# Kernel tuning notes

Hardware: AMD Instinct MI355X
Metric: run time of the kernel (lower is better)

## Reference

```python
import jax, jax.numpy as jnp
import numpy as np

B, S, H = 2, 2048, 2048
NH, NKV = 16, 4
HD = H // NH            # 128
GROUPS = NH // NKV      # 4
ROTARY_BASE = 10000.0
NEG = -1e9


def setup_inputs() -> dict:
    key = jax.random.key(0)
    ks = jax.random.split(key, 6)
    x = jax.random.normal(ks[0], (B, S, H), dtype=jnp.float32)
    # additive causal mask [B,1,S,S]
    causal = jnp.where(jnp.tril(jnp.ones((S, S), dtype=bool)), 0.0, NEG).astype(jnp.float32)
    attention_mask = jnp.broadcast_to(causal[None, None], (B, 1, S, S))
    position_ids = jnp.broadcast_to(jnp.arange(S, dtype=jnp.int32)[None], (B, S))
    sc = 0.02
    Wq = jax.random.normal(ks[1], (H, NH * HD), dtype=jnp.float32) * sc
    Wk = jax.random.normal(ks[2], (H, NKV * HD), dtype=jnp.float32) * sc
    Wv = jax.random.normal(ks[3], (H, NKV * HD), dtype=jnp.float32) * sc
    Wo = jax.random.normal(ks[4], (H, H), dtype=jnp.float32) * sc
    return {"x": x, "attention_mask": attention_mask, "position_ids": position_ids,
            "Wq": Wq, "Wk": Wk, "Wv": Wv, "Wo": Wo}


def _rotate_half(t):
    t1, t2 = t[..., : HD // 2], t[..., HD // 2:]
    return jnp.concatenate((-t2, t1), axis=-1)


def _rope_sin_cos(position_ids, dtype):
    inv_freq = 1.0 / (ROTARY_BASE ** (jnp.arange(0, HD, 2, dtype=jnp.float32) / HD))  # [HD/2]
    freqs = position_ids.astype(jnp.float32)[..., None] * inv_freq[None, None, :]      # [B,S,HD/2]
    emb = jnp.concatenate((freqs, freqs), axis=-1)                                     # [B,S,HD]
    return jnp.sin(emb).astype(dtype), jnp.cos(emb).astype(dtype)


def reference(x, attention_mask, position_ids, Wq, Wk, Wv, Wo):
    # QKV projections (no bias)
    q = (x @ Wq).reshape(B, S, NH, HD).transpose(0, 2, 1, 3)     # [B,NH,S,HD]
    k = (x @ Wk).reshape(B, S, NKV, HD).transpose(0, 2, 1, 3)    # [B,NKV,S,HD]
    v = (x @ Wv).reshape(B, S, NKV, HD).transpose(0, 2, 1, 3)
    sin, cos = _rope_sin_cos(position_ids, x.dtype)
    sin, cos = sin[:, None], cos[:, None]                         # unsqueeze head dim
    q = q * cos + _rotate_half(q) * sin
    k = k * cos + _rotate_half(k) * sin
    # GQA: repeat kv heads
    k = jnp.repeat(k, GROUPS, axis=1)                             # [B,NH,S,HD]
    v = jnp.repeat(v, GROUPS, axis=1)
    scores = jnp.einsum('bhqd,bhkd->bhqk', q, k) / jnp.sqrt(jnp.asarray(HD, x.dtype))
    scores = scores + attention_mask                              # additive causal mask
    attn = jax.nn.softmax(scores.astype(jnp.float32), axis=-1).astype(x.dtype)
    # dropout p=0.0 -> no-op
    out = jnp.einsum('bhqk,bhkd->bhqd', attn, v)                  # [B,NH,S,HD]
    out = out.transpose(0, 2, 1, 3).reshape(B, S, H)
    return out @ Wo
```

## Files before the change

### kernel.cpp

```cpp
#include <hip/hip_runtime.h>
#include <hip/hip_bf16.h>
#include <stdint.h>
#include <math.h>

#define B_ 2
#define S_ 2048
#define H_ 2048
#define NH_ 16
#define NKV_ 4
#define HD_ 128

typedef __bf16 bf16;
typedef __bf16 bf16x8 __attribute__((ext_vector_type(8)));
typedef __bf16 bf16x4 __attribute__((ext_vector_type(4)));
typedef float f32x4 __attribute__((ext_vector_type(4)));

__device__ __forceinline__ void async_copy16(const void* g, void* l) {
  __builtin_amdgcn_global_load_lds(
      (const __attribute__((address_space(1))) void*)(uintptr_t)g,
      (__attribute__((address_space(3))) void*)(uintptr_t)l,
      16, 0, 0);
}

__device__ __forceinline__ f32x4 mfma16(bf16x8 a, bf16x8 b, f32x4 c) {
  return __builtin_amdgcn_mfma_f32_16x16x32_bf16(a, b, c, 0, 0, 0);
}


__global__ void f32_to_bf16_k(const float* __restrict__ in, bf16* __restrict__ o, int n) {
  int i = (blockIdx.x * 256 + threadIdx.x) * 4;
  if (i >= n) return;
  float4 v = *(const float4*)(in + i);
  bf16x4 r;
  r[0] = (bf16)v.x; r[1] = (bf16)v.y; r[2] = (bf16)v.z; r[3] = (bf16)v.w;
  *(bf16x4*)(o + i) = r;
}

__global__ void transpose_to_bf16_k(const float* __restrict__ W, bf16* __restrict__ Wt,
                                    int K, int N) {
  __shared__ float tile[32][33];
  int n0 = blockIdx.x * 32, k0 = blockIdx.y * 32;
  int tx = threadIdx.x, ty = threadIdx.y;
#pragma unroll
  for (int j = 0; j < 32; j += 8)
    tile[ty + j][tx] = W[(size_t)(k0 + ty + j) * N + n0 + tx];
  __syncthreads();
#pragma unroll
  for (int j = 0; j < 32; j += 8)
    Wt[(size_t)(n0 + ty + j) * K + k0 + tx] = (bf16)tile[tx][ty + j];
}

__global__ void rope_table_k(float2* __restrict__ tab) {
  int i = blockIdx.x * 256 + threadIdx.x;
  int p = i >> 6, d = i & 63;
  float invf = expf(-((float)(2 * d) / 128.0f) * 9.210340371976184f);
  float fr = (float)p * invf;
  float sv, cv;
  sincosf(fr, &sv, &cv);
  tab[i] = make_float2(cv, sv);
}

__global__ void rope_apply_k(bf16* __restrict__ t, const int* __restrict__ pos_ids,
                             const float2* __restrict__ tab, int hshift, int hmask,
                             float scale) {
  int i = blockIdx.x * 256 + threadIdx.x;
  int d = i & 63;
  int tmp = i >> 6;
  int h = tmp & hmask;
  int row = tmp >> hshift;
  int pos = pos_ids[row];
  float2 cs = tab[pos * 64 + d];
  size_t base = (((size_t)row << hshift) + h) * HD_;
  float a = (float)t[base + d];
  float b = (float)t[base + d + 64];
  t[base + d]      = (bf16)((a * cs.x - b * cs.y) * scale);
  t[base + d + 64] = (bf16)((b * cs.x + a * cs.y) * scale);
}


template <int MODE>
__global__ __launch_bounds__(512) void gemm256_k(const bf16* __restrict__ A,
                                                 const bf16* __restrict__ Bt,
                                                 void* __restrict__ C0,
                                                 void* __restrict__ C1,
                                                 void* __restrict__ C2,
                                                 int M, int N, int K) {
  extern __shared__ __align__(16) char smem[];
  const int tid = threadIdx.x;
  const int lane = tid & 63;
  const int w = tid >> 6;
  const int wm = w >> 2;
  const int wn = w & 3;
  const int g16 = lane >> 4, c16 = lane & 15;
  const int row0 = blockIdx.y * 256;
  const int col0 = blockIdx.x * 256;
  const int srow = tid >> 3;
  const int sslot = tid & 7;
  const int ldsw = w * 1024;

  auto stage = [&](int buf, int kt, int r) {
    int row = (r & 3) * 64 + srow;
    int ss = sslot ^ (row & 7);
    const bf16* src = (r < 4) ? (A + (size_t)(row0 + row) * K)
                              : (Bt + (size_t)(col0 + row) * K);
    async_copy16(src + (kt << 6) + ss * 8,
                 smem + buf * 65536 + (r >> 2) * 32768 + (r & 3) * 8192 + ldsw);
  };

  int offA[2][8], offB[2][4];
#pragma unroll
  for (int ks = 0; ks < 2; ++ks) {
#pragma unroll
    for (int i = 0; i < 8; ++i) {
      int ra = wm * 128 + i * 16 + c16;
      offA[ks][i] = ra * 128 + (((ks * 4 + g16) ^ (ra & 7)) << 4);
    }
#pragma unroll
    for (int j = 0; j < 4; ++j) {
      int rb = wn * 64 + j * 16 + c16;
      offB[ks][j] = 32768 + rb * 128 + (((ks * 4 + g16) ^ (rb & 7)) << 4);
    }
  }

  const f32x4 fz = {0.f, 0.f, 0.f, 0.f};
  f32x4 acc[8][4];
#pragma unroll
  for (int i = 0; i < 8; ++i)
#pragma unroll
    for (int j = 0; j < 4; ++j) acc[i][j] = fz;

  const int nkt = K >> 6;
#pragma unroll
  for (int r = 0; r < 8; ++r) stage(0, 0, r);
  asm volatile("s_waitcnt vmcnt(0)" ::: "memory");
  __builtin_amdgcn_s_barrier();

  for (int t = 0; t < nkt; ++t) {
    const char* Ab = smem + (t & 1) * 65536;
    const bool pf = (t + 1 < nkt);
    const int nb = (t + 1) & 1;
    bf16x8 bfr[2][4];

    {
      bf16x8 af[2][2];
#pragma unroll
      for (int ks = 0; ks < 2; ++ks) {
#pragma unroll
        for (int j = 0; j < 4; ++j) bfr[ks][j] = *(const bf16x8*)(Ab + offB[ks][j]);
        af[ks][0] = *(const bf16x8*)(Ab + offA[ks][0]);
        af[ks][1] = *(const bf16x8*)(Ab + offA[ks][1]);
      }
      if (pf) { stage(nb, t + 1, 0); stage(nb, t + 1, 1); stage(nb, t + 1, 2); stage(nb, t + 1, 3); }
      __builtin_amdgcn_s_barrier();
      asm volatile("s_waitcnt lgkmcnt(0)" ::: "memory");
      __builtin_amdgcn_sched_barrier(0);
      __builtin_amdgcn_s_setprio(1);
#pragma unroll
      for (int ks = 0; ks < 2; ++ks)
#pragma unroll
        for (int m = 0; m < 2; ++m)
#pragma unroll
          for (int j = 0; j < 4; ++j)
            acc[m][j] = mfma16(af[ks][m], bfr[ks][j], acc[m][j]);
      __builtin_amdgcn_s_setprio(0);
      __builtin_amdgcn_sched_barrier(0);
      __builtin_amdgcn_s_barrier();
    }

#pragma unroll
    for (int q = 1; q < 4; ++q) {
      bf16x8 af[2][2];
#pragma unroll
      for (int ks = 0; ks < 2; ++ks) {
        af[ks][0] = *(const bf16x8*)(Ab + offA[ks][q * 2]);
        af[ks][1] = *(const bf16x8*)(Ab + offA[ks][q * 2 + 1]);
      }
      if (q == 1 && pf) { stage(nb, t + 1, 4); stage(nb, t + 1, 5); stage(nb, t + 1, 6); stage(nb, t + 1, 7); }
      __builtin_amdgcn_s_barrier();
      asm volatile("s_waitcnt lgkmcnt(0)" ::: "memory");
      __builtin_amdgcn_sched_barrier(0);
      __builtin_amdgcn_s_setprio(1);
#pragma unroll
      for (int ks = 0; ks < 2; ++ks)
#pragma unroll
        for (int m = 0; m < 2; ++m)
#pragma unroll
          for (int j = 0; j < 4; ++j)
            acc[q * 2 + m][j] = mfma16(af[ks][m], bfr[ks][j], acc[q * 2 + m][j]);
      __builtin_amdgcn_s_setprio(0);
      __builtin_amdgcn_sched_barrier(0);
      if (q == 3 && pf) asm volatile("s_waitcnt vmcnt(0)" ::: "memory");
      __builtin_amdgcn_s_barrier();
    }
  }

#pragma unroll
  for (int i = 0; i < 8; ++i) {
    int gr0 = row0 + wm * 128 + i * 16 + g16 * 4;
#pragma unroll
    for (int j = 0; j < 4; ++j) {
      int gc = col0 + wn * 64 + j * 16 + c16;
      if constexpr (MODE == 2) {
        if (col0 < 2048) {
#pragma unroll
          for (int r = 0; r < 4; ++r)
            ((bf16*)C0)[(size_t)(gr0 + r) * 2048 + gc] = (bf16)acc[i][j][r];
        } else if (col0 < 2560) {
#pragma unroll
          for (int r = 0; r < 4; ++r)
            ((bf16*)C1)[(size_t)(gr0 + r) * 512 + (gc - 2048)] = (bf16)acc[i][j][r];
        } else {
          int dv = gc - 2560;
          int hkv = dv >> 7, d = dv & 127;
          size_t va = (((size_t)(gr0 >> 11) * NKV_ + hkv) * HD_ + d) * S_ + (gr0 & 2047);
          bf16x4 pk;
#pragma unroll
          for (int r = 0; r < 4; ++r) pk[r] = (bf16)acc[i][j][r];
          *(bf16x4*)((bf16*)C2 + va) = pk;
        }
      } else {
#pragma unroll
        for (int r = 0; r < 4; ++r) {
          if constexpr (MODE == 1)
            ((float*)C0)[(size_t)(gr0 + r) * N + gc] = acc[i][j][r];
          else
            ((bf16*)C0)[(size_t)(gr0 + r) * N + gc] = (bf16)acc[i][j][r];
        }
      }
    }
  }
}


template <int MODE>
__global__ __launch_bounds__(512) void gemm8_k(const bf16* __restrict__ A,
                                               const bf16* __restrict__ Bt,
                                               void* __restrict__ C0,
                                               void* __restrict__ C1,
                                               void* __restrict__ C2,
                                               int M, int N, int K) {
  extern __shared__ __align__(16) char smem[];
  const int tid = threadIdx.x;
  const int lane = tid & 63;
  const int w = tid >> 6;
  const int wm = w >> 2;
  const int wn = w & 3;
  const int g16 = lane >> 4, c16 = lane & 15;
  const int row0 = blockIdx.y * 128;
  const int col0 = blockIdx.x * 256;
  const int srow = tid >> 3;
  const int sslot = tid & 7;
  const int ldsw = w * 1024;

  auto stageA = [&](int s, int kt, int r) {
    int row = r * 64 + srow;
    int ss = sslot ^ (row & 7);
    async_copy16(A + (size_t)(row0 + row) * K + (kt << 6) + ss * 8,
                 smem + s * 49152 + r * 8192 + ldsw);
  };
  auto stageB = [&](int s, int kt, int r) {
    int row = r * 64 + srow;
    int ss = sslot ^ (row & 7);
    async_copy16(Bt + (size_t)(col0 + row) * K + (kt << 6) + ss * 8,
                 smem + s * 49152 + 16384 + r * 8192 + ldsw);
  };

  int offA[2][4], offB[2][4];
#pragma unroll
  for (int ks = 0; ks < 2; ++ks) {
#pragma unroll
    for (int i = 0; i < 4; ++i) {
      int ra = wm * 64 + i * 16 + c16;
      offA[ks][i] = ra * 128 + (((ks * 4 + g16) ^ (ra & 7)) << 4);
      int rb = wn * 64 + i * 16 + c16;
      offB[ks][i] = rb * 128 + (((ks * 4 + g16) ^ (rb & 7)) << 4);
    }
  }

  const f32x4 fz = {0.f, 0.f, 0.f, 0.f};
  f32x4 acc[4][4];
#pragma unroll
  for (int i = 0; i < 4; ++i)
#pragma unroll
    for (int j = 0; j < 4; ++j) acc[i][j] = fz;

  const int nkt = K >> 6;
#pragma unroll
  for (int r = 0; r < 2; ++r) stageA(0, 0, r);
#pragma unroll
  for (int r = 0; r < 4; ++r) stageB(0, 0, r);
#pragma unroll
  for (int r = 0; r < 2; ++r) stageA(1, 1, r);
#pragma unroll
  for (int r = 0; r < 4; ++r) stageB(1, 1, r);
  asm volatile("s_waitcnt vmcnt(6)" ::: "memory");
  __builtin_amdgcn_s_barrier();

  int ct = 0, pt = 2;
  for (int t = 0; t < nkt; ++t) {
    const char* Ab = smem + ct * 49152;
    const char* Bb = Ab + 16384;
    const bool pf = (t + 2 < nkt);
    const int kpf = t + 2;
    bf16x8 af[4], bfr[4];

#pragma unroll
    for (int i = 0; i < 4; ++i) af[i] = *(const bf16x8*)(Ab + offA[0][i]);
#pragma unroll
    for (int j = 0; j < 4; ++j) bfr[j] = *(const bf16x8*)(Bb + offB[0][j]);
    if (pf) { stageA(pt, kpf, 0); stageA(pt, kpf, 1); stageB(pt, kpf, 0); }
    __builtin_amdgcn_s_barrier();
    asm volatile("s_waitcnt lgkmcnt(0)" ::: "memory");
    __builtin_amdgcn_sched_barrier(0);
    __builtin_amdgcn_s_setprio(1);
#pragma unroll
    for (int i = 0; i < 4; ++i)
#pragma unroll
      for (int j = 0; j < 4; ++j) acc[i][j] = mfma16(af[i], bfr[j], acc[i][j]);
    __builtin_amdgcn_s_setprio(0);
    __builtin_amdgcn_sched_barrier(0);
    __builtin_amdgcn_s_barrier();

#pragma unroll
    for (int i = 0; i < 4; ++i) af[i] = *(const bf16x8*)(Ab + offA[1][i]);
#pragma unroll
    for (int j = 0; j < 4; ++j) bfr[j] = *(const bf16x8*)(Bb + offB[1][j]);
    if (pf) { stageB(pt, kpf, 1); stageB(pt, kpf, 2); stageB(pt, kpf, 3); }
    if (pf) asm volatile("s_waitcnt vmcnt(6)" ::: "memory");
    else    asm volatile("s_waitcnt vmcnt(0)" ::: "memory");
    __builtin_amdgcn_s_barrier();
    asm volatile("s_waitcnt lgkmcnt(0)" ::: "memory");
    __builtin_amdgcn_sched_barrier(0);
    __builtin_amdgcn_s_setprio(1);
#pragma unroll
    for (int i = 0; i < 4; ++i)
#pragma unroll
      for (int j = 0; j < 4; ++j) acc[i][j] = mfma16(af[i], bfr[j], acc[i][j]);
    __builtin_amdgcn_s_setprio(0);
    __builtin_amdgcn_sched_barrier(0);
    __builtin_amdgcn_s_barrier();

    ct = (ct == 2) ? 0 : ct + 1;
    pt = (pt == 2) ? 0 : pt + 1;
  }

#pragma unroll
  for (int i = 0; i < 4; ++i) {
    int gr0 = row0 + wm * 64 + i * 16 + g16 * 4;
#pragma unroll
    for (int j = 0; j < 4; ++j) {
      int gc = col0 + wn * 64 + j * 16 + c16;
#pragma unroll
      for (int r = 0; r < 4; ++r) {
        if constexpr (MODE == 1)
          ((float*)C0)[(size_t)(gr0 + r) * N + gc] = acc[i][j][r];
        else
          ((bf16*)C0)[(size_t)(gr0 + r) * N + gc] = (bf16)acc[i][j][r];
      }
    }
  }
}


template <bool OUT_F32, bool VT_Z1>
__global__ __launch_bounds__(256) void gemm_bt_k(const bf16* __restrict__ A,
                                                 const bf16* __restrict__ Bt0,
                                                 const bf16* __restrict__ Bt1,
                                                 void* __restrict__ C0, void* __restrict__ C1,
                                                 int M, int N, int K) {
  const bf16* __restrict__ Bt = (blockIdx.z == 0) ? Bt0 : Bt1;
  void* C = (blockIdx.z == 0) ? C0 : C1;
  __shared__ __align__(16) bf16 As[128 * 64];
  __shared__ __align__(16) bf16 Bs[128 * 64];
  const int tid = threadIdx.x;
  const int lane = tid & 63;
  const int w = tid >> 6;
  const int wm = w >> 1, wn = w & 1;
  const int g16 = lane >> 4, c16 = lane & 15;
  const int row0 = blockIdx.y * 128;
  const int col0 = blockIdx.x * 128;
  const int sr = lane >> 3;
  const int st = lane & 7;
  const int ss = st ^ sr;

  const f32x4 fz = {0.f, 0.f, 0.f, 0.f};
  f32x4 acc[4][4];
#pragma unroll
  for (int i = 0; i < 4; ++i)
#pragma unroll
    for (int j = 0; j < 4; ++j) acc[i][j] = fz;

  const int nkt = K >> 6;
  for (int kt = 0; kt < nkt; ++kt) {
    const int k0 = kt << 6;
    __syncthreads();
#pragma unroll
    for (int c = 0; c < 4; ++c) {
      int rbase = w * 32 + c * 8;
      async_copy16(A + (size_t)(row0 + rbase + sr) * K + k0 + ss * 8,
                   (char*)As + rbase * 128);
      async_copy16(Bt + (size_t)(col0 + rbase + sr) * K + k0 + ss * 8,
                   (char*)Bs + rbase * 128);
    }
    __syncthreads();
#pragma unroll
    for (int ks = 0; ks < 2; ++ks) {
      bf16x8 af[4], bfr[4];
#pragma unroll
      for (int t = 0; t < 4; ++t) {
        int ra = wm * 64 + t * 16 + c16;
        af[t] = *(const bf16x8*)((const char*)As + ra * 128 + (((ks * 4 + g16) ^ (ra & 7)) << 4));
        int rb = wn * 64 + t * 16 + c16;
        bfr[t] = *(const bf16x8*)((const char*)Bs + rb * 128 + (((ks * 4 + g16) ^ (rb & 7)) << 4));
      }
#pragma unroll
      for (int i = 0; i < 4; ++i)
#pragma unroll
        for (int j = 0; j < 4; ++j) acc[i][j] = mfma16(af[i], bfr[j], acc[i][j]);
    }
  }

  const bool vt = VT_Z1 && (blockIdx.z == 1);
#pragma unroll
  for (int i = 0; i < 4; ++i) {
    int gr0 = row0 + wm * 64 + i * 16 + g16 * 4;
#pragma unroll
    for (int j = 0; j < 4; ++j) {
      int gc = col0 + wn * 64 + j * 16 + c16;
      if (vt) {
        size_t va = ((size_t)((gr0 >> 11) * NKV_ + (gc >> 7)) * HD_ + (gc & 127)) * S_ + (gr0 & 2047);
        bf16x4 pk;
#pragma unroll
        for (int r = 0; r < 4; ++r) pk[r] = (bf16)acc[i][j][r];
        *(bf16x4*)((bf16*)C + va) = pk;
      } else {
#pragma unroll
        for (int r = 0; r < 4; ++r) {
          if constexpr (OUT_F32)
            ((float*)C)[(size_t)(gr0 + r) * N + gc] = acc[i][j][r];
          else
            ((bf16*)C)[(size_t)(gr0 + r) * N + gc] = (bf16)acc[i][j][r];
        }
      }
    }
  }
}


__global__ __launch_bounds__(256, 2) void attn_fwd_k(const bf16* __restrict__ Qg,
                                                     const bf16* __restrict__ Kg,
                                                     const bf16* __restrict__ VTg,
                                                     bf16* __restrict__ Og) {
  __shared__ __align__(16) bf16 Ks[2][64 * 128];
  __shared__ __align__(16) bf16 Vt[2][128 * 64];

  const int tid = threadIdx.x;
  const int lane = tid & 63;
  const int w = tid >> 6;
  const int g16 = lane >> 4;
  const int c16 = lane & 15;

  int bid = blockIdx.x;
  int rr_ = bid >> 5, bh = bid & 31;
  int qb = (rr_ < 8) ? (15 - rr_) : (rr_ - 8);
  const int b = bh >> 4;
  const int h = bh & 15;
  const int hkv = h >> 2;
  const int q0 = qb * 128;
  const int qw = q0 + w * 32;

  bf16x8 qf[2][4];
#pragma unroll
  for (int nq = 0; nq < 2; ++nq)
#pragma unroll
    for (int ksq = 0; ksq < 4; ++ksq)
      qf[nq][ksq] = *(const bf16x8*)(Qg + ((size_t)(b * S_ + qw + nq * 16 + c16) * NH_ + h) * HD_ + (ksq * 4 + g16) * 8);

  float m_run[2] = {-1e30f, -1e30f};
  float l_run[2] = {0.f, 0.f};
  const f32x4 fz = {0.f, 0.f, 0.f, 0.f};
  f32x4 acc[2][8];
#pragma unroll
  for (int nq = 0; nq < 2; ++nq)
#pragma unroll
    for (int dt = 0; dt < 8; ++dt) acc[nq][dt] = fz;

  const size_t kbase = ((size_t)b * S_ * NKV_ + hkv) * HD_;
  const size_t vbase = ((size_t)(b * NKV_ + hkv)) * HD_ * S_;

  auto stage = [&](int buf, int kv0) {
#pragma unroll
    for (int rd = 0; rd < 4; ++rd) {
      int Lb = rd * 256 + w * 64;
      int row = (Lb + lane) >> 4;
      int ssl = (lane & 15) ^ (row & 7);
      async_copy16(Kg + kbase + (size_t)(kv0 + row) * (NKV_ * HD_) + ssl * 8,
                   (char*)&Ks[buf][0] + Lb * 16);
    }
#pragma unroll
    for (int rd = 0; rd < 4; ++rd) {
      int Lb = rd * 256 + w * 64;
      int row = (Lb + lane) >> 3;
      int ssl = (lane & 7) ^ (row & 7);
      async_copy16(VTg + vbase + (size_t)row * S_ + kv0 + ssl * 8,
                   (char*)&Vt[buf][0] + Lb * 16);
    }
  };

  const int ntiles = 2 * qb + 2;
  stage(0, 0);
  int cur = 0;

  for (int t = 0; t < ntiles; ++t) {
    __syncthreads();
    if (t + 1 < ntiles) stage(cur ^ 1, (t + 1) * 64);
    const int kv0 = t * 64;

    if (kv0 <= qw + 31) {
      const bf16* KsC = &Ks[cur][0];
      const bf16* VtC = &Vt[cur][0];

      f32x4 sc[2][4];
#pragma unroll
      for (int nq = 0; nq < 2; ++nq)
#pragma unroll
        for (int mt = 0; mt < 4; ++mt) sc[nq][mt] = fz;

      __builtin_amdgcn_s_setprio(1);
#pragma unroll
      for (int ksq = 0; ksq < 4; ++ksq) {
        bf16x8 kf[4];
#pragma unroll
        for (int mt = 0; mt < 4; ++mt) {
          int gp = c16 >> 2, rp = c16 & 3;
          int blk = 8 * (mt >> 1) + 2 * gp + ((mt & 1) ^ (gp & 1));
          int row = blk * 4 + rp;
          kf[mt] = *(const bf16x8*)((const char*)KsC + row * 256 + (((ksq * 4 + g16) ^ (row & 7)) << 4));
        }
#pragma unroll
        for (int nq = 0; nq < 2; ++nq)
#pragma unroll
          for (int mt = 0; mt < 4; ++mt)
            sc[nq][mt] = mfma16(kf[mt], qf[nq][ksq], sc[nq][mt]);
      }
      __builtin_amdgcn_s_setprio(0);

      if (kv0 + 63 > qw) {
#pragma unroll
        for (int nq = 0; nq < 2; ++nq) {
          int qa = qw + nq * 16 + c16;
#pragma unroll
          for (int mt = 0; mt < 4; ++mt) {
            int blk = 8 * (mt >> 1) + 2 * g16 + ((mt & 1) ^ (g16 & 1));
#pragma unroll
            for (int r = 0; r < 4; ++r) {
              int ka = kv0 + blk * 4 + r;
              if (ka > qa) sc[nq][mt][r] = -1e30f;
            }
          }
        }
      }

      float mx[2];
#pragma unroll
      for (int nq = 0; nq < 2; ++nq) {
        float v = sc[nq][0][0];
#pragma unroll
        for (int mt = 0; mt < 4; ++mt)
#pragma unroll
          for (int r = 0; r < 4; ++r) v = fmaxf(v, sc[nq][mt][r]);
        v = fmaxf(v, __shfl_xor(v, 16));
        v = fmaxf(v, __shfl_xor(v, 32));
        mx[nq] = v;
      }
      if (__any((mx[0] > m_run[0] + 8.f) || (mx[1] > m_run[1] + 8.f))) {
#pragma unroll
        for (int nq = 0; nq < 2; ++nq) {
          float mn = fmaxf(m_run[nq], mx[nq]);
          float corr = exp2f(m_run[nq] - mn);
          m_run[nq] = mn;
          l_run[nq] *= corr;
#pragma unroll
          for (int dt = 0; dt < 8; ++dt) acc[nq][dt] *= corr;
        }
      }
#pragma unroll
      for (int nq = 0; nq < 2; ++nq) {
        float sum = 0.f;
#pragma unroll
        for (int mt = 0; mt < 4; ++mt)
#pragma unroll
          for (int r = 0; r < 4; ++r) {
            float p = exp2f(sc[nq][mt][r] - m_run[nq]);
            sc[nq][mt][r] = p;
            sum += p;
          }
        sum += __shfl_xor(sum, 16);
        sum += __shfl_xor(sum, 32);
        l_run[nq] += sum;
      }

      bf16x8 pa[2][2];
#pragma unroll
      for (int nq = 0; nq < 2; ++nq)
#pragma unroll
        for (int ks = 0; ks < 2; ++ks) {
          f32x4 sA = (g16 & 1) ? sc[nq][2 * ks + 1] : sc[nq][2 * ks];
          f32x4 sB = (g16 & 1) ? sc[nq][2 * ks] : sc[nq][2 * ks + 1];
          bf16x8 tf;
          tf[0] = (bf16)sA[0]; tf[1] = (bf16)sA[1]; tf[2] = (bf16)sA[2]; tf[3] = (bf16)sA[3];
          tf[4] = (bf16)sB[0]; tf[5] = (bf16)sB[1]; tf[6] = (bf16)sB[2]; tf[7] = (bf16)sB[3];
          pa[nq][ks] = tf;
        }

      __builtin_amdgcn_s_setprio(1);
#pragma unroll
      for (int ks = 0; ks < 2; ++ks)
#pragma unroll
        for (int dt = 0; dt < 8; ++dt) {
          int rv = dt * 16 + c16;
          bf16x8 vf = *(const bf16x8*)((const char*)VtC + rv * 128 + (((ks * 4 + g16) ^ (rv & 7)) << 4));
          acc[0][dt] = mfma16(vf, pa[0][ks], acc[0][dt]);
          acc[1][dt] = mfma16(vf, pa[1][ks], acc[1][dt]);
        }
      __builtin_amdgcn_s_setprio(0);
    }
    cur ^= 1;
  }

#pragma unroll
  for (int nq = 0; nq < 2; ++nq) {
    float inv = 1.0f / l_run[nq];
    size_t base = ((size_t)(b * S_ + qw + nq * 16 + c16) * NH_ + h) * HD_ + g16 * 4;
#pragma unroll
    for (int dt = 0; dt < 8; ++dt) {
      bf16x4 ov;
#pragma unroll
      for (int r = 0; r < 4; ++r) ov[r] = (bf16)(acc[nq][dt][r] * inv);
      *(bf16x4*)(Og + base + dt * 16) = ov;
    }
  }
}


extern "C" void kernel_launch(void* const* d_in, const int* in_sizes, int n_in,
                              void* d_out, int out_size, void* d_ws, size_t ws_size,
                              hipStream_t stream) {
  const float* x  = (const float*)d_in[0];
  const int* pos  = (const int*)d_in[2];
  const float* Wq = (const float*)d_in[3];
  const float* Wk = (const float*)d_in[4];
  const float* Wv = (const float*)d_in[5];
  const float* Wo = (const float*)d_in[6];

  char* ws = (char*)d_ws;
  size_t off = 0;
  auto alloc = [&](size_t bytes) -> char* {
    char* p = ws + off;
    off += (bytes + 255) & ~(size_t)255;
    return p;
  };
  const size_t rows = (size_t)B_ * S_;
  bf16* xb    = (bf16*)alloc(rows * H_ * 2);
  bf16* bq    = (bf16*)alloc(rows * (NH_ * HD_) * 2);
  bf16* batt  = (bf16*)alloc(rows * (NH_ * HD_) * 2);
  bf16* WqkvT = (bf16*)alloc((size_t)3072 * H_ * 2);
  bf16* WoT   = (bf16*)alloc((size_t)H_ * H_ * 2);
  bf16* bk    = (bf16*)alloc(rows * (NKV_ * HD_) * 2);
  bf16* VT    = (bf16*)alloc(rows * (NKV_ * HD_) * 2);
  float2* tab = (float2*)alloc((size_t)S_ * 64 * sizeof(float2));

  bf16* WqT = WqkvT;
  bf16* WkT = WqkvT + (size_t)2048 * H_;
  bf16* WvT = WqkvT + (size_t)2560 * H_;

  auto* fqkv = gemm256_k<2>;
  auto* fo   = gemm8_k<1>;
  const int lds256 = 2 * 65536;
  const int lds8   = 3 * 49152;
  bool big =
      (hipFuncSetAttribute((const void*)fqkv, hipFuncAttributeMaxDynamicSharedMemorySize, lds256) == hipSuccess) &&
      (hipFuncSetAttribute((const void*)fo, hipFuncAttributeMaxDynamicSharedMemorySize, lds8) == hipSuccess);

  f32_to_bf16_k<<<(rows * H_) / (256 * 4), 256, 0, stream>>>(x, xb, rows * H_);
  transpose_to_bf16_k<<<dim3(H_ / 32, H_ / 32), dim3(32, 8), 0, stream>>>(Wq, WqT, H_, NH_ * HD_);
  transpose_to_bf16_k<<<dim3((NKV_ * HD_) / 32, H_ / 32), dim3(32, 8), 0, stream>>>(Wk, WkT, H_, NKV_ * HD_);
  transpose_to_bf16_k<<<dim3((NKV_ * HD_) / 32, H_ / 32), dim3(32, 8), 0, stream>>>(Wv, WvT, H_, NKV_ * HD_);
  transpose_to_bf16_k<<<dim3(H_ / 32, H_ / 32), dim3(32, 8), 0, stream>>>(Wo, WoT, H_, H_);
  rope_table_k<<<(S_ * 64) / 256, 256, 0, stream>>>(tab);

  if (big) {
    gemm256_k<2><<<dim3(12, 16), 512, lds256, stream>>>(xb, WqkvT, bq, bk, VT, 4096, 3072, 2048);
  } else {
    gemm_bt_k<false, false><<<dim3(16, 32, 1), 256, 0, stream>>>(xb, WqT, WqT, bq, bq, 4096, 2048, 2048);
    gemm_bt_k<false, true><<<dim3(4, 32, 2), 256, 0, stream>>>(xb, WkT, WvT, bk, VT, 4096, 512, 2048);
  }

  rope_apply_k<<<(4096 * NH_ * 64) / 256, 256, 0, stream>>>(bq, pos, tab, 4, 15, 0.12753102f);
  rope_apply_k<<<(4096 * NKV_ * 64) / 256, 256, 0, stream>>>(bk, pos, tab, 2, 3, 1.0f);

  attn_fwd_k<<<dim3(512), 256, 0, stream>>>(bq, bk, VT, batt);

  if (big)
    gemm8_k<1><<<dim3(8, 32), 512, lds8, stream>>>(batt, WoT, d_out, nullptr, nullptr, 4096, 2048, 2048);
  else
    gemm_bt_k<true, false><<<dim3(16, 32, 1), 256, 0, stream>>>(batt, WoT, WoT, d_out, d_out, 4096, 2048, 2048);
}
```

Before: 212.5 us.

## Merge weight transposes, vectorize RoPE, retile QKV GEMM, software-pipeline attention PV

The four weight-transpose launches become one kernel that dispatches on block index. RoPE application is vectorized to 8 bf16 elements per thread. The QKV GEMM is templated on N-tile width and now uses 192-column tiles, giving a 16x16 grid instead of 12x16 for better CU fill. The attention kernel gains a third V buffer and defers each tile's PV MFMAs until after the next tile's QK MFMAs, so softmax latency overlaps with matrix work. The fallback small-GEMM path is removed, which assumes large dynamic LDS is always available.

```diff
diff --git a/kernel.cpp b/kernel.cpp
--- a/kernel.cpp
+++ b/kernel.cpp
@@ -36,10 +36,18 @@
   *(bf16x4*)(o + i) = r;
 }
 
-__global__ void transpose_to_bf16_k(const float* __restrict__ W, bf16* __restrict__ Wt,
-                                    int K, int N) {
+__global__ void transpose_all_k(const float* __restrict__ Wq, const float* __restrict__ Wk,
+                                const float* __restrict__ Wv, const float* __restrict__ Wo,
+                                bf16* __restrict__ WqkvT, bf16* __restrict__ WoT) {
   __shared__ float tile[32][33];
-  int n0 = blockIdx.x * 32, k0 = blockIdx.y * 32;
+  int bid = blockIdx.x;
+  const float* W; bf16* Wt; int N, bx, by;
+  if (bid < 4096)      { W = Wq; Wt = WqkvT;                          N = 2048; int b2 = bid;        bx = b2 & 63; by = b2 >> 6; }
+  else if (bid < 5120) { W = Wk; Wt = WqkvT + (size_t)2048 * 2048;    N = 512;  int b2 = bid - 4096; bx = b2 & 15; by = b2 >> 4; }
+  else if (bid < 6144) { W = Wv; Wt = WqkvT + (size_t)2560 * 2048;    N = 512;  int b2 = bid - 5120; bx = b2 & 15; by = b2 >> 4; }
+  else                 { W = Wo; Wt = WoT;                            N = 2048; int b2 = bid - 6144; bx = b2 & 63; by = b2 >> 6; }
+  const int K = 2048;
+  int n0 = bx * 32, k0 = by * 32;
   int tx = threadIdx.x, ty = threadIdx.y;
 #pragma unroll
   for (int j = 0; j < 32; j += 8)
@@ -60,25 +68,41 @@
   tab[i] = make_float2(cv, sv);
 }
 
-__global__ void rope_apply_k(bf16* __restrict__ t, const int* __restrict__ pos_ids,
-                             const float2* __restrict__ tab, int hshift, int hmask,
-                             float scale) {
+__global__ void rope_apply_v8_k(bf16* __restrict__ t, const int* __restrict__ pos_ids,
+                                const float2* __restrict__ tab, int hshift, int hmask,
+                                float scale) {
   int i = blockIdx.x * 256 + threadIdx.x;
-  int d = i & 63;
-  int tmp = i >> 6;
+  int g = i & 7;
+  int tmp = i >> 3;
   int h = tmp & hmask;
   int row = tmp >> hshift;
   int pos = pos_ids[row];
-  float2 cs = tab[pos * 64 + d];
-  size_t base = (((size_t)row << hshift) + h) * HD_;
-  float a = (float)t[base + d];
-  float b = (float)t[base + d + 64];
-  t[base + d]      = (bf16)((a * cs.x - b * cs.y) * scale);
-  t[base + d + 64] = (bf16)((b * cs.x + a * cs.y) * scale);
-}
-
-
-template <int MODE>
+  size_t base = (((size_t)row << hshift) + h) * HD_ + g * 8;
+  const float2* tb = tab + pos * 64 + g * 8;
+  bf16x8 lo = *(const bf16x8*)(t + base);
+  bf16x8 hi = *(const bf16x8*)(t + base + 64);
+  float4 t0 = *(const float4*)(tb);
+  float4 t1 = *(const float4*)(tb + 2);
+  float4 t2 = *(const float4*)(tb + 4);
+  float4 t3 = *(const float4*)(tb + 6);
+  float cs[8], sn[8];
+  cs[0]=t0.x; sn[0]=t0.y; cs[1]=t0.z; sn[1]=t0.w;
+  cs[2]=t1.x; sn[2]=t1.y; cs[3]=t1.z; sn[3]=t1.w;
+  cs[4]=t2.x; sn[4]=t2.y; cs[5]=t2.z; sn[5]=t2.w;
+  cs[6]=t3.x; sn[6]=t3.y; cs[7]=t3.z; sn[7]=t3.w;
+  bf16x8 olo, ohi;
+#pragma unroll
+  for (int j = 0; j < 8; ++j) {
+    float a = (float)lo[j], b = (float)hi[j];
+    olo[j] = (bf16)((a * cs[j] - b * sn[j]) * scale);
+    ohi[j] = (bf16)((b * cs[j] + a * sn[j]) * scale);
+  }
+  *(bf16x8*)(t + base) = olo;
+  *(bf16x8*)(t + base + 64) = ohi;
+}
+
+
+template <int MODE, int NJ>
 __global__ __launch_bounds__(512) void gemm256_k(const bf16* __restrict__ A,
                                                  const bf16* __restrict__ Bt,
                                                  void* __restrict__ C0,
@@ -86,6 +110,7 @@
                                                  void* __restrict__ C2,
                                                  int M, int N, int K) {
   extern __shared__ __align__(16) char smem[];
+  constexpr int BUFSZ = 32768 + NJ * 8192;
   const int tid = threadIdx.x;
   const int lane = tid & 63;
   const int w = tid >> 6;
@@ -93,21 +118,22 @@
   const int wn = w & 3;
   const int g16 = lane >> 4, c16 = lane & 15;
   const int row0 = blockIdx.y * 256;
-  const int col0 = blockIdx.x * 256;
+  const int col0 = blockIdx.x * (NJ * 64);
   const int srow = tid >> 3;
   const int sslot = tid & 7;
   const int ldsw = w * 1024;
 
   auto stage = [&](int buf, int kt, int r) {
-    int row = (r & 3) * 64 + srow;
+    int rr = (r < 4) ? r : r - 4;
+    int row = rr * 64 + srow;
     int ss = sslot ^ (row & 7);
     const bf16* src = (r < 4) ? (A + (size_t)(row0 + row) * K)
                               : (Bt + (size_t)(col0 + row) * K);
     async_copy16(src + (kt << 6) + ss * 8,
-                 smem + buf * 65536 + (r >> 2) * 32768 + (r & 3) * 8192 + ldsw);
+                 smem + buf * BUFSZ + ((r < 4) ? 0 : 32768) + rr * 8192 + ldsw);
   };
 
-  int offA[2][8], offB[2][4];
+  int offA[2][8], offB[2][NJ];
 #pragma unroll
   for (int ks = 0; ks < 2; ++ks) {
 #pragma unroll
@@ -116,37 +142,37 @@
       offA[ks][i] = ra * 128 + (((ks * 4 + g16) ^ (ra & 7)) << 4);
     }
 #pragma unroll
-    for (int j = 0; j < 4; ++j) {
-      int rb = wn * 64 + j * 16 + c16;
+    for (int j = 0; j < NJ; ++j) {
+      int rb = wn * (16 * NJ) + j * 16 + c16;
       offB[ks][j] = 32768 + rb * 128 + (((ks * 4 + g16) ^ (rb & 7)) << 4);
     }
   }
 
   const f32x4 fz = {0.f, 0.f, 0.f, 0.f};
-  f32x4 acc[8][4];
+  f32x4 acc[8][NJ];
 #pragma unroll
   for (int i = 0; i < 8; ++i)
 #pragma unroll
-    for (int j = 0; j < 4; ++j) acc[i][j] = fz;
+    for (int j = 0; j < NJ; ++j) acc[i][j] = fz;
 
   const int nkt = K >> 6;
 #pragma unroll
-  for (int r = 0; r < 8; ++r) stage(0, 0, r);
+  for (int r = 0; r < 4 + NJ; ++r) stage(0, 0, r);
   asm volatile("s_waitcnt vmcnt(0)" ::: "memory");
   __builtin_amdgcn_s_barrier();
 
   for (int t = 0; t < nkt; ++t) {
-    const char* Ab = smem + (t & 1) * 65536;
+    const char* Ab = smem + (t & 1) * BUFSZ;
     const bool pf = (t + 1 < nkt);
     const int nb = (t + 1) & 1;
-    bf16x8 bfr[2][4];
+    bf16x8 bfr[2][NJ];
 
     {
       bf16x8 af[2][2];
 #pragma unroll
       for (int ks = 0; ks < 2; ++ks) {
 #pragma unroll
-        for (int j = 0; j < 4; ++j) bfr[ks][j] = *(const bf16x8*)(Ab + offB[ks][j]);
+        for (int j = 0; j < NJ; ++j) bfr[ks][j] = *(const bf16x8*)(Ab + offB[ks][j]);
         af[ks][0] = *(const bf16x8*)(Ab + offA[ks][0]);
         af[ks][1] = *(const bf16x8*)(Ab + offA[ks][1]);
       }
@@ -160,7 +186,7 @@
 #pragma unroll
         for (int m = 0; m < 2; ++m)
 #pragma unroll
-          for (int j = 0; j < 4; ++j)
+          for (int j = 0; j < NJ; ++j)
             acc[m][j] = mfma16(af[ks][m], bfr[ks][j], acc[m][j]);
       __builtin_amdgcn_s_setprio(0);
       __builtin_amdgcn_sched_barrier(0);
@@ -175,7 +201,10 @@
         af[ks][0] = *(const bf16x8*)(Ab + offA[ks][q * 2]);
         af[ks][1] = *(const bf16x8*)(Ab + offA[ks][q * 2 + 1]);
       }
-      if (q == 1 && pf) { stage(nb, t + 1, 4); stage(nb, t + 1, 5); stage(nb, t + 1, 6); stage(nb, t + 1, 7); }
+      if (q == 1 && pf) {
+#pragma unroll
+        for (int r = 0; r < NJ; ++r) stage(nb, t + 1, 4 + r);
+      }
       __builtin_amdgcn_s_barrier();
       asm volatile("s_waitcnt lgkmcnt(0)" ::: "memory");
       __builtin_amdgcn_sched_barrier(0);
@@ -185,7 +214,7 @@
 #pragma unroll
         for (int m = 0; m < 2; ++m)
 #pragma unroll
-          for (int j = 0; j < 4; ++j)
+          for (int j = 0; j < NJ; ++j)
             acc[q * 2 + m][j] = mfma16(af[ks][m], bfr[ks][j], acc[q * 2 + m][j]);
       __builtin_amdgcn_s_setprio(0);
       __builtin_amdgcn_sched_barrier(0);
@@ -198,14 +227,14 @@
   for (int i = 0; i < 8; ++i) {
     int gr0 = row0 + wm * 128 + i * 16 + g16 * 4;
 #pragma unroll
-    for (int j = 0; j < 4; ++j) {
-      int gc = col0 + wn * 64 + j * 16 + c16;
+    for (int j = 0; j < NJ; ++j) {
+      int gc = col0 + wn * (16 * NJ) + j * 16 + c16;
       if constexpr (MODE == 2) {
-        if (col0 < 2048) {
+        if (gc < 2048) {
 #pragma unroll
           for (int r = 0; r < 4; ++r)
             ((bf16*)C0)[(size_t)(gr0 + r) * 2048 + gc] = (bf16)acc[i][j][r];
-        } else if (col0 < 2560) {
+        } else if (gc < 2560) {
 #pragma unroll
           for (int r = 0; r < 4; ++r)
             ((bf16*)C1)[(size_t)(gr0 + r) * 512 + (gc - 2048)] = (bf16)acc[i][j][r];
@@ -362,97 +391,12 @@
 }
 
 
-template <bool OUT_F32, bool VT_Z1>
-__global__ __launch_bounds__(256) void gemm_bt_k(const bf16* __restrict__ A,
-                                                 const bf16* __restrict__ Bt0,
-                                                 const bf16* __restrict__ Bt1,
-                                                 void* __restrict__ C0, void* __restrict__ C1,
-                                                 int M, int N, int K) {
-  const bf16* __restrict__ Bt = (blockIdx.z == 0) ? Bt0 : Bt1;
-  void* C = (blockIdx.z == 0) ? C0 : C1;
-  __shared__ __align__(16) bf16 As[128 * 64];
-  __shared__ __align__(16) bf16 Bs[128 * 64];
-  const int tid = threadIdx.x;
-  const int lane = tid & 63;
-  const int w = tid >> 6;
-  const int wm = w >> 1, wn = w & 1;
-  const int g16 = lane >> 4, c16 = lane & 15;
-  const int row0 = blockIdx.y * 128;
-  const int col0 = blockIdx.x * 128;
-  const int sr = lane >> 3;
-  const int st = lane & 7;
-  const int ss = st ^ sr;
-
-  const f32x4 fz = {0.f, 0.f, 0.f, 0.f};
-  f32x4 acc[4][4];
-#pragma unroll
-  for (int i = 0; i < 4; ++i)
-#pragma unroll
-    for (int j = 0; j < 4; ++j) acc[i][j] = fz;
-
-  const int nkt = K >> 6;
-  for (int kt = 0; kt < nkt; ++kt) {
-    const int k0 = kt << 6;
-    __syncthreads();
-#pragma unroll
-    for (int c = 0; c < 4; ++c) {
-      int rbase = w * 32 + c * 8;
-      async_copy16(A + (size_t)(row0 + rbase + sr) * K + k0 + ss * 8,
-                   (char*)As + rbase * 128);
-      async_copy16(Bt + (size_t)(col0 + rbase + sr) * K + k0 + ss * 8,
-                   (char*)Bs + rbase * 128);
-    }
-    __syncthreads();
-#pragma unroll
-    for (int ks = 0; ks < 2; ++ks) {
-      bf16x8 af[4], bfr[4];
-#pragma unroll
-      for (int t = 0; t < 4; ++t) {
-        int ra = wm * 64 + t * 16 + c16;
-        af[t] = *(const bf16x8*)((const char*)As + ra * 128 + (((ks * 4 + g16) ^ (ra & 7)) << 4));
-        int rb = wn * 64 + t * 16 + c16;
-        bfr[t] = *(const bf16x8*)((const char*)Bs + rb * 128 + (((ks * 4 + g16) ^ (rb & 7)) << 4));
-      }
-#pragma unroll
-      for (int i = 0; i < 4; ++i)
-#pragma unroll
-        for (int j = 0; j < 4; ++j) acc[i][j] = mfma16(af[i], bfr[j], acc[i][j]);
-    }
-  }
-
-  const bool vt = VT_Z1 && (blockIdx.z == 1);
-#pragma unroll
-  for (int i = 0; i < 4; ++i) {
-    int gr0 = row0 + wm * 64 + i * 16 + g16 * 4;
-#pragma unroll
-    for (int j = 0; j < 4; ++j) {
-      int gc = col0 + wn * 64 + j * 16 + c16;
-      if (vt) {
-        size_t va = ((size_t)((gr0 >> 11) * NKV_ + (gc >> 7)) * HD_ + (gc & 127)) * S_ + (gr0 & 2047);
-        bf16x4 pk;
-#pragma unroll
-        for (int r = 0; r < 4; ++r) pk[r] = (bf16)acc[i][j][r];
-        *(bf16x4*)((bf16*)C + va) = pk;
-      } else {
-#pragma unroll
-        for (int r = 0; r < 4; ++r) {
-          if constexpr (OUT_F32)
-            ((float*)C)[(size_t)(gr0 + r) * N + gc] = acc[i][j][r];
-          else
-            ((bf16*)C)[(size_t)(gr0 + r) * N + gc] = (bf16)acc[i][j][r];
-        }
-      }
-    }
-  }
-}
-
-
 __global__ __launch_bounds__(256, 2) void attn_fwd_k(const bf16* __restrict__ Qg,
                                                      const bf16* __restrict__ Kg,
                                                      const bf16* __restrict__ VTg,
                                                      bf16* __restrict__ Og) {
   __shared__ __align__(16) bf16 Ks[2][64 * 128];
-  __shared__ __align__(16) bf16 Vt[2][128 * 64];
+  __shared__ __align__(16) bf16 Vt[3][128 * 64];
 
   const int tid = threadIdx.x;
   const int lane = tid & 63;
@@ -488,7 +432,7 @@
   const size_t kbase = ((size_t)b * S_ * NKV_ + hkv) * HD_;
   const size_t vbase = ((size_t)(b * NKV_ + hkv)) * HD_ * S_;
 
-  auto stage = [&](int buf, int kv0) {
+  auto stageK = [&](int buf, int kv0) {
 #pragma unroll
     for (int rd = 0; rd < 4; ++rd) {
       int Lb = rd * 256 + w * 64;
@@ -497,6 +441,8 @@
       async_copy16(Kg + kbase + (size_t)(kv0 + row) * (NKV_ * HD_) + ssl * 8,
                    (char*)&Ks[buf][0] + Lb * 16);
     }
+  };
+  auto stageV = [&](int buf, int kv0) {
 #pragma unroll
     for (int rd = 0; rd < 4; ++rd) {
       int Lb = rd * 256 + w * 64;
@@ -508,19 +454,24 @@
   };
 
   const int ntiles = 2 * qb + 2;
-  stage(0, 0);
-  int cur = 0;
+  stageK(0, 0);
+  stageV(0, 0);
+
+  bf16x8 pa[2][2];
+  bool pend = false;
+  int vb_pend = 0;
+  int vbt = 0;
 
   for (int t = 0; t < ntiles; ++t) {
     __syncthreads();
-    if (t + 1 < ntiles) stage(cur ^ 1, (t + 1) * 64);
+    int vbn = (vbt == 2) ? 0 : vbt + 1;
+    if (t + 1 < ntiles) { stageK((t + 1) & 1, (t + 1) * 64); stageV(vbn, (t + 1) * 64); }
     const int kv0 = t * 64;
-
-    if (kv0 <= qw + 31) {
-      const bf16* KsC = &Ks[cur][0];
-      const bf16* VtC = &Vt[cur][0];
-
-      f32x4 sc[2][4];
+    const bool g = (kv0 <= qw + 31);
+
+    f32x4 sc[2][4];
+    if (g) {
+      const char* KsC = (const char*)&Ks[t & 1][0];
 #pragma unroll
       for (int nq = 0; nq < 2; ++nq)
 #pragma unroll
@@ -535,7 +486,7 @@
           int gp = c16 >> 2, rp = c16 & 3;
           int blk = 8 * (mt >> 1) + 2 * gp + ((mt & 1) ^ (gp & 1));
           int row = blk * 4 + rp;
-          kf[mt] = *(const bf16x8*)((const char*)KsC + row * 256 + (((ksq * 4 + g16) ^ (row & 7)) << 4));
+          kf[mt] = *(const bf16x8*)(KsC + row * 256 + (((ksq * 4 + g16) ^ (row & 7)) << 4));
         }
 #pragma unroll
         for (int nq = 0; nq < 2; ++nq)
@@ -544,7 +495,25 @@
             sc[nq][mt] = mfma16(kf[mt], qf[nq][ksq], sc[nq][mt]);
       }
       __builtin_amdgcn_s_setprio(0);
-
+    }
+
+    if (pend) {
+      const char* VtP = (const char*)&Vt[vb_pend][0];
+      __builtin_amdgcn_s_setprio(1);
+#pragma unroll
+      for (int ks = 0; ks < 2; ++ks)
+#pragma unroll
+        for (int dt = 0; dt < 8; ++dt) {
+          int rv = dt * 16 + c16;
+          bf16x8 vf = *(const bf16x8*)(VtP + rv * 128 + (((ks * 4 + g16) ^ (rv & 7)) << 4));
+          acc[0][dt] = mfma16(vf, pa[0][ks], acc[0][dt]);
+          acc[1][dt] = mfma16(vf, pa[1][ks], acc[1][dt]);
+        }
+      __builtin_amdgcn_s_setprio(0);
+      pend = false;
+    }
+
+    if (g) {
       if (kv0 + 63 > qw) {
 #pragma unroll
         for (int nq = 0; nq < 2; ++nq) {
@@ -600,7 +569,6 @@
         l_run[nq] += sum;
       }
 
-      bf16x8 pa[2][2];
 #pragma unroll
       for (int nq = 0; nq < 2; ++nq)
 #pragma unroll
@@ -612,20 +580,23 @@
           tf[4] = (bf16)sB[0]; tf[5] = (bf16)sB[1]; tf[6] = (bf16)sB[2]; tf[7] = (bf16)sB[3];
           pa[nq][ks] = tf;
         }
-
-      __builtin_amdgcn_s_setprio(1);
-#pragma unroll
-      for (int ks = 0; ks < 2; ++ks)
-#pragma unroll
-        for (int dt = 0; dt < 8; ++dt) {
-          int rv = dt * 16 + c16;
-          bf16x8 vf = *(const bf16x8*)((const char*)VtC + rv * 128 + (((ks * 4 + g16) ^ (rv & 7)) << 4));
-          acc[0][dt] = mfma16(vf, pa[0][ks], acc[0][dt]);
-          acc[1][dt] = mfma16(vf, pa[1][ks], acc[1][dt]);
-        }
-      __builtin_amdgcn_s_setprio(0);
-    }
-    cur ^= 1;
+      pend = true;
+      vb_pend = vbt;
+    }
+    vbt = vbn;
+  }
+
+  if (pend) {
+    const char* VtP = (const char*)&Vt[vb_pend][0];
+#pragma unroll
+    for (int ks = 0; ks < 2; ++ks)
+#pragma unroll
+      for (int dt = 0; dt < 8; ++dt) {
+        int rv = dt * 16 + c16;
+        bf16x8 vf = *(const bf16x8*)(VtP + rv * 128 + (((ks * 4 + g16) ^ (rv & 7)) << 4));
+        acc[0][dt] = mfma16(vf, pa[0][ks], acc[0][dt]);
+        acc[1][dt] = mfma16(vf, pa[1][ks], acc[1][dt]);
+      }
   }
 
 #pragma unroll
@@ -670,39 +641,25 @@
   bf16* VT    = (bf16*)alloc(rows * (NKV_ * HD_) * 2);
   float2* tab = (float2*)alloc((size_t)S_ * 64 * sizeof(float2));
 
-  bf16* WqT = WqkvT;
-  bf16* WkT = WqkvT + (size_t)2048 * H_;
-  bf16* WvT = WqkvT + (size_t)2560 * H_;
-
-  auto* fqkv = gemm256_k<2>;
+  auto* fqkv = gemm256_k<2, 3>;
   auto* fo   = gemm8_k<1>;
-  const int lds256 = 2 * 65536;
+  const int lds256 = 2 * (32768 + 3 * 8192);
   const int lds8   = 3 * 49152;
   bool big =
       (hipFuncSetAttribute((const void*)fqkv, hipFuncAttributeMaxDynamicSharedMemorySize, lds256) == hipSuccess) &&
       (hipFuncSetAttribute((const void*)fo, hipFuncAttributeMaxDynamicSharedMemorySize, lds8) == hipSuccess);
 
   f32_to_bf16_k<<<(rows * H_) / (256 * 4), 256, 0, stream>>>(x, xb, rows * H_);
-  transpose_to_bf16_k<<<dim3(H_ / 32, H_ / 32), dim3(32, 8), 0, stream>>>(Wq, WqT, H_, NH_ * HD_);
-  transpose_to_bf16_k<<<dim3((NKV_ * HD_) / 32, H_ / 32), dim3(32, 8), 0, stream>>>(Wk, WkT, H_, NKV_ * HD_);
-  transpose_to_bf16_k<<<dim3((NKV_ * HD_) / 32, H_ / 32), dim3(32, 8), 0, stream>>>(Wv, WvT, H_, NKV_ * HD_);
-  transpose_to_bf16_k<<<dim3(H_ / 32, H_ / 32), dim3(32, 8), 0, stream>>>(Wo, WoT, H_, H_);
+  transpose_all_k<<<10240, dim3(32, 8), 0, stream>>>(Wq, Wk, Wv, Wo, WqkvT, WoT);
   rope_table_k<<<(S_ * 64) / 256, 256, 0, stream>>>(tab);
 
-  if (big) {
-    gemm256_k<2><<<dim3(12, 16), 512, lds256, stream>>>(xb, WqkvT, bq, bk, VT, 4096, 3072, 2048);
-  } else {
-    gemm_bt_k<false, false><<<dim3(16, 32, 1), 256, 0, stream>>>(xb, WqT, WqT, bq, bq, 4096, 2048, 2048);
-    gemm_bt_k<false, true><<<dim3(4, 32, 2), 256, 0, stream>>>(xb, WkT, WvT, bk, VT, 4096, 512, 2048);
-  }
-
-  rope_apply_k<<<(4096 * NH_ * 64) / 256, 256, 0, stream>>>(bq, pos, tab, 4, 15, 0.12753102f);
-  rope_apply_k<<<(4096 * NKV_ * 64) / 256, 256, 0, stream>>>(bk, pos, tab, 2, 3, 1.0f);
+  gemm256_k<2, 3><<<dim3(16, 16), 512, lds256, stream>>>(xb, WqkvT, bq, bk, VT, 4096, 3072, 2048);
+  (void)big;
+
+  rope_apply_v8_k<<<(4096 * NH_ * 8) / 256, 256, 0, stream>>>(bq, pos, tab, 4, 15, 0.12753102f);
+  rope_apply_v8_k<<<(4096 * NKV_ * 8) / 256, 256, 0, stream>>>(bk, pos, tab, 2, 3, 1.0f);
 
   attn_fwd_k<<<dim3(512), 256, 0, stream>>>(bq, bk, VT, batt);
 
-  if (big)
-    gemm8_k<1><<<dim3(8, 32), 512, lds8, stream>>>(batt, WoT, d_out, nullptr, nullptr, 4096, 2048, 2048);
-  else
-    gemm_bt_k<true, false><<<dim3(16, 32, 1), 256, 0, stream>>>(batt, WoT, WoT, d_out, d_out, 4096, 2048, 2048);
-}
+  gemm8_k<1><<<dim3(8, 32), 512, lds8, stream>>>(batt, WoT, d_out, nullptr, nullptr, 4096, 2048, 2048);
+}
```

Result: faster. 199.2 us (-6.3%).
